# Optimization experiments

Hardware: AMD Instinct MI355X
Metric: run time of the kernel (lower is better)

The kernel has to match this reference:

```python
import jax, jax.numpy as jnp
import numpy as np

B, S, D, H = 4, 2048, 1024, 16
DH = D // H


def setup_inputs() -> dict:
    key = jax.random.key(0)
    ks = jax.random.split(key, 7)
    return {
        "Q": jax.random.normal(ks[0], (B, S, D), dtype=jnp.float32),
        "K": jax.random.normal(ks[1], (B, S, D), dtype=jnp.float32),
        "V": jax.random.normal(ks[2], (B, S, D), dtype=jnp.float32),
        "q_proj": jax.random.normal(ks[3], (D, D), dtype=jnp.float32),
        "k_proj": jax.random.normal(ks[4], (D, D), dtype=jnp.float32),
        "v_proj": jax.random.normal(ks[5], (D, D), dtype=jnp.float32),
        "output_proj": jax.random.normal(ks[6], (D, D), dtype=jnp.float32),
        "casual": 1,
    }


def reference(Q, K, V, q_proj, k_proj, v_proj, output_proj, casual):
    # projections: einsum('... a b, ... s b -> ... s a') == x @ W.T
    q = jnp.einsum('bsd,ad->bsa', Q, q_proj)
    k = jnp.einsum('bsd,ad->bsa', K, k_proj)
    v = jnp.einsum('bsd,ad->bsa', V, v_proj)
    # split heads: [B, S, H, DH]
    q = q.reshape(B, S, H, DH)
    k = k.reshape(B, S, H, DH)
    v = v.reshape(B, S, H, DH)
    # scores [B, H, Sq, Sk]
    scores = jnp.einsum('bqhd,bkhd->bhqk', q, k) / np.sqrt(DH).astype(np.float32)
    # causal mask: 0 on lower triangle, -inf above
    causal_mask = jnp.where(
        jnp.tril(jnp.ones((S, S), dtype=bool)), 0.0, -jnp.inf
    ).astype(scores.dtype)
    scores = scores + causal_mask
    attn = jax.nn.softmax(scores, axis=-1)
    # weighted values -> [B, Sq, H, DH] -> [B, Sq, D]
    out = jnp.einsum('bhqk,bkhd->bqhd', attn, v).reshape(B, S, D)
    # output projection: einsum('... a b, ... b -> ... a') == x @ W.T
    return jnp.einsum('bsd,ad->bsa', out, output_proj)
```

## Files before the change

kernel.cpp:

```cpp
#include <hip/hip_runtime.h>


typedef __attribute__((ext_vector_type(8))) _Float16 half8;
typedef __attribute__((ext_vector_type(4))) float f32x4;

#define DEVI static __device__ __forceinline__

static constexpr int cB = 4, cS = 2048, cD = 1024, cH = 16, cDH = 64;
static constexpr int cM = cB * cS;

DEVI unsigned short h2b(_Float16 h) { union { _Float16 f; unsigned short u; } x; x.f = h; return x.u; }

DEVI void async16(const void* g, void* l) {
#if defined(__HIP_DEVICE_COMPILE__)
  __builtin_amdgcn_global_load_lds((const __attribute__((address_space(1))) unsigned int*)g,
                                   (__attribute__((address_space(3))) unsigned int*)l, 16, 0, 0);
#endif
}

__global__ void split_f16_kernel(const float* __restrict__ in, unsigned short* __restrict__ hi,
                                 unsigned short* __restrict__ lo, int n) {
  int i = (blockIdx.x * blockDim.x + threadIdx.x) * 4;
  if (i >= n) return;
  float4 v = *(const float4*)(in + i);
  _Float16 h0 = (_Float16)v.x, h1 = (_Float16)v.y, h2 = (_Float16)v.z, h3 = (_Float16)v.w;
  unsigned short th[4] = {h2b(h0), h2b(h1), h2b(h2), h2b(h3)};
  *(uint2*)(hi + i) = *(const uint2*)th;
  if (lo != nullptr) {
    unsigned short tl[4] = {h2b((_Float16)(v.x - (float)h0)), h2b((_Float16)(v.y - (float)h1)),
                            h2b((_Float16)(v.z - (float)h2)), h2b((_Float16)(v.w - (float)h3))};
    *(uint2*)(lo + i) = *(const uint2*)tl;
  }
}

template <int PASSES, int OUTMODE, bool A32>
__global__ __launch_bounds__(256, 2) void gemm_bt(const void* __restrict__ Ap,
                                                  const unsigned short* __restrict__ Bh,
                                                  const unsigned short* __restrict__ Bl,
                                                  void* __restrict__ C0, void* __restrict__ C1,
                                                  int M, int N, int K) {
  __shared__ float sA32[A32 ? 128 * 32 : 1];
  __shared__ unsigned short sA16[A32 ? 1 : 128 * 32];
  __shared__ unsigned short sBh[128 * 32];
  __shared__ unsigned short sBl[(PASSES == 3) ? 128 * 32 : 1];

  const int tid = threadIdx.x, lane = tid & 63, wave = tid >> 6;
  const int wm = wave >> 1, wn = wave & 1;
  const int nb = N >> 7;
  const int bm = blockIdx.x / nb, bn = blockIdx.x % nb;
  const long r0 = (long)bm * 128, c0 = (long)bn * 128;
  const int quad = lane >> 4, cl = lane & 15;

  f32x4 acc[4][4];
#pragma unroll
  for (int mt = 0; mt < 4; ++mt)
#pragma unroll
    for (int nt = 0; nt < 4; ++nt) acc[mt][nt] = f32x4{0.f, 0.f, 0.f, 0.f};

  const int lrow8 = lane >> 3, lg8 = lane & 7;
  const int lrow16 = lane >> 2, lg4 = lane & 3;

  const float* A32p = (const float*)Ap;
  const unsigned short* A16p = (const unsigned short*)Ap;

  for (int k0 = 0; k0 < K; k0 += 32) {
    __syncthreads();
    if constexpr (A32) {
#pragma unroll
      for (int c = 0; c < 4; ++c) {
        int cc = wave * 4 + c;
        int r = cc * 8 + lrow8;
        const float* g = A32p + (r0 + r) * (long)K + k0 + ((lg8 ^ lrow8) * 4);
        async16(g, sA32 + cc * 256);
      }
    } else {
#pragma unroll
      for (int c = 0; c < 2; ++c) {
        int cc = wave * 2 + c;
        int r = cc * 16 + lrow16;
        const unsigned short* g =
            A16p + (r0 + r) * (long)K + k0 + ((lg4 ^ ((lrow16 >> 1) & 3)) * 8);
        async16(g, sA16 + cc * 512);
      }
    }
#pragma unroll
    for (int c = 0; c < 2; ++c) {
      int cc = wave * 2 + c;
      int r = cc * 16 + lrow16;
      long gb = (c0 + r) * (long)K + k0 + ((lg4 ^ ((lrow16 >> 1) & 3)) * 8);
      async16(Bh + gb, sBh + cc * 512);
      if constexpr (PASSES == 3) async16(Bl + gb, sBl + cc * 512);
    }
    __syncthreads();

    half8 ah[4], al[4], bh8[4], bl8[4];
    if constexpr (A32) {
#pragma unroll
      for (int mt = 0; mt < 4; ++mt) {
        int r = wm * 64 + mt * 16 + cl;
        int s0 = (quad * 2 + 0) ^ (r & 7), s1 = (quad * 2 + 1) ^ (r & 7);
        float fa[8];
        *(float4*)(fa) = *(const float4*)(sA32 + r * 32 + s0 * 4);
        *(float4*)(fa + 4) = *(const float4*)(sA32 + r * 32 + s1 * 4);
#pragma unroll
        for (int j = 0; j < 8; ++j) {
          _Float16 h = (_Float16)fa[j];
          ah[mt][j] = h;
          if constexpr (PASSES == 3) al[mt][j] = (_Float16)(fa[j] - (float)h);
        }
      }
    } else {
#pragma unroll
      for (int mt = 0; mt < 4; ++mt) {
        int r = wm * 64 + mt * 16 + cl;
        int s = quad ^ ((r >> 1) & 3);
        ah[mt] = *(const half8*)(sA16 + r * 32 + s * 8);
      }
    }
#pragma unroll
    for (int nt = 0; nt < 4; ++nt) {
      int r = wn * 64 + nt * 16 + cl;
      int s = quad ^ ((r >> 1) & 3);
      bh8[nt] = *(const half8*)(sBh + r * 32 + s * 8);
      if constexpr (PASSES == 3) bl8[nt] = *(const half8*)(sBl + r * 32 + s * 8);
    }
#pragma unroll
    for (int mt = 0; mt < 4; ++mt)
#pragma unroll
      for (int nt = 0; nt < 4; ++nt) {
        acc[mt][nt] = __builtin_amdgcn_mfma_f32_16x16x32_f16(ah[mt], bh8[nt], acc[mt][nt], 0, 0, 0);
        if constexpr (PASSES == 3) {
          acc[mt][nt] = __builtin_amdgcn_mfma_f32_16x16x32_f16(ah[mt], bl8[nt], acc[mt][nt], 0, 0, 0);
          acc[mt][nt] = __builtin_amdgcn_mfma_f32_16x16x32_f16(al[mt], bh8[nt], acc[mt][nt], 0, 0, 0);
        }
      }
  }

#pragma unroll
  for (int mt = 0; mt < 4; ++mt)
#pragma unroll
    for (int nt = 0; nt < 4; ++nt)
#pragma unroll
      for (int i = 0; i < 4; ++i) {
        long row = r0 + wm * 64 + mt * 16 + quad * 4 + i;
        long col = c0 + wn * 64 + nt * 16 + cl;
        float v = acc[mt][nt][i];
        if constexpr (OUTMODE == 2) {
          ((float*)C0)[row * N + col] = v;
        } else if constexpr (OUTMODE == 0) {
          ((unsigned short*)C0)[row * N + col] = h2b((_Float16)v);
        } else {
          _Float16 h = (_Float16)v;
          ((unsigned short*)C0)[row * N + col] = h2b(h);
          ((unsigned short*)C1)[row * N + col] = h2b((_Float16)(v - (float)h));
        }
      }
}

__global__ __launch_bounds__(256, 2) void flash_kernel(
    const unsigned short* __restrict__ qh_g, const unsigned short* __restrict__ ql_g,
    const unsigned short* __restrict__ kh_g, const unsigned short* __restrict__ kl_g,
    const unsigned short* __restrict__ vp_g, unsigned short* __restrict__ out) {
  __shared__ unsigned short sKh[64 * 64];
  __shared__ unsigned short sKl[64 * 64];
  __shared__ unsigned short sVt[64 * 72];
  __shared__ unsigned short sP[4][32 * 40];

  const int tid = threadIdx.x, lane = tid & 63, wave = tid >> 6;
  const int quad = lane >> 4, cl = lane & 15;
  const int qt = blockIdx.x & 15;
  const int h = (blockIdx.x >> 4) & 15;
  const int b = blockIdx.x >> 8;
  const long rowbase = (long)b * cS;
  const int q0 = qt * 128;

  half8 qh[2][2], ql[2][2];
#pragma unroll
  for (int ks = 0; ks < 2; ++ks)
#pragma unroll
    for (int mt = 0; mt < 2; ++mt) {
      long r = rowbase + q0 + wave * 32 + mt * 16 + cl;
      long off = r * cD + h * 64 + ks * 32 + quad * 8;
      qh[ks][mt] = *(const half8*)(qh_g + off);
      ql[ks][mt] = *(const half8*)(ql_g + off);
    }

  f32x4 O[2][4];
  float mrow[2][4], lrow[2][4];
#pragma unroll
  for (int mt = 0; mt < 2; ++mt) {
#pragma unroll
    for (int dt = 0; dt < 4; ++dt) O[mt][dt] = f32x4{0.f, 0.f, 0.f, 0.f};
#pragma unroll
    for (int i = 0; i < 4; ++i) { mrow[mt][i] = -1e30f; lrow[mt][i] = 0.f; }
  }

  const int lrow8 = lane >> 3, lg8 = lane & 7;
  const int kimax = 2 * qt + 1;
  for (int ki = 0; ki <= kimax; ++ki) {
    __syncthreads();
#pragma unroll
    for (int c = 0; c < 2; ++c) {
      int cc = wave * 2 + c;
      int r = cc * 8 + lrow8;
      long g = (rowbase + ki * 64 + r) * (long)cD + h * 64 + ((lg8 ^ lrow8) * 8);
      async16(kh_g + g, sKh + cc * 512);
      async16(kl_g + g, sKl + cc * 512);
    }
    {
      int r = tid >> 2, dh0 = (tid & 3) * 16;
      const unsigned short* gv = vp_g + (rowbase + ki * 64 + r) * (long)cD + h * 64 + dh0;
      unsigned short buf[16];
      *(uint4*)(buf) = *(const uint4*)(gv);
      *(uint4*)(buf + 8) = *(const uint4*)(gv + 8);
#pragma unroll
      for (int j = 0; j < 16; ++j) sVt[(dh0 + j) * 72 + r] = buf[j];
    }
    __syncthreads();

    f32x4 sacc[2][4];
#pragma unroll
    for (int mt = 0; mt < 2; ++mt)
#pragma unroll
      for (int nt = 0; nt < 4; ++nt) sacc[mt][nt] = f32x4{0.f, 0.f, 0.f, 0.f};
#pragma unroll
    for (int ks = 0; ks < 2; ++ks) {
      half8 kh8[4], kl8[4];
#pragma unroll
      for (int nt = 0; nt < 4; ++nt) {
        int r = nt * 16 + cl;
        int off = r * 64 + (((ks * 4 + quad) ^ (r & 7)) * 8);
        kh8[nt] = *(const half8*)(sKh + off);
        kl8[nt] = *(const half8*)(sKl + off);
      }
#pragma unroll
      for (int mt = 0; mt < 2; ++mt)
#pragma unroll
        for (int nt = 0; nt < 4; ++nt) {
          sacc[mt][nt] = __builtin_amdgcn_mfma_f32_16x16x32_f16(qh[ks][mt], kh8[nt], sacc[mt][nt], 0, 0, 0);
          sacc[mt][nt] = __builtin_amdgcn_mfma_f32_16x16x32_f16(qh[ks][mt], kl8[nt], sacc[mt][nt], 0, 0, 0);
          sacc[mt][nt] = __builtin_amdgcn_mfma_f32_16x16x32_f16(ql[ks][mt], kh8[nt], sacc[mt][nt], 0, 0, 0);
        }
    }
    const bool need_mask = (ki >= 2 * qt);
#pragma unroll
    for (int mt = 0; mt < 2; ++mt)
#pragma unroll
      for (int nt = 0; nt < 4; ++nt)
#pragma unroll
        for (int i = 0; i < 4; ++i) {
          float s = sacc[mt][nt][i] * 0.125f;
          if (need_mask) {
            int rg = q0 + wave * 32 + mt * 16 + quad * 4 + i;
            int cg = ki * 64 + nt * 16 + cl;
            if (cg > rg) s = -1e30f;
          }
          sacc[mt][nt][i] = s;
        }
    float alpha[2][4];
#pragma unroll
    for (int mt = 0; mt < 2; ++mt)
#pragma unroll
      for (int i = 0; i < 4; ++i) {
        float mx = sacc[mt][0][i];
#pragma unroll
        for (int nt = 1; nt < 4; ++nt) mx = fmaxf(mx, sacc[mt][nt][i]);
#pragma unroll
        for (int d = 1; d < 16; d <<= 1) mx = fmaxf(mx, __shfl_xor(mx, d));
        float mnew = fmaxf(mrow[mt][i], mx);
        float a = __expf(mrow[mt][i] - mnew);
        mrow[mt][i] = mnew;
        alpha[mt][i] = a;
        float rs = 0.f;
#pragma unroll
        for (int nt = 0; nt < 4; ++nt) {
          float p = __expf(sacc[mt][nt][i] - mnew);
          sacc[mt][nt][i] = p;
          rs += p;
        }
#pragma unroll
        for (int d = 1; d < 16; d <<= 1) rs += __shfl_xor(rs, d);
        lrow[mt][i] = lrow[mt][i] * a + rs;
      }
#pragma unroll
    for (int mt = 0; mt < 2; ++mt)
#pragma unroll
      for (int dt = 0; dt < 4; ++dt)
#pragma unroll
        for (int i = 0; i < 4; ++i) O[mt][dt][i] *= alpha[mt][i];

    unsigned short* sPw = sP[wave];
#pragma unroll
    for (int kc = 0; kc < 2; ++kc) {
#pragma unroll
      for (int mt = 0; mt < 2; ++mt)
#pragma unroll
        for (int ntl = 0; ntl < 2; ++ntl) {
          int nt = kc * 2 + ntl;
#pragma unroll
          for (int i = 0; i < 4; ++i)
            sPw[(mt * 16 + quad * 4 + i) * 40 + ntl * 16 + cl] = h2b((_Float16)sacc[mt][nt][i]);
        }
      half8 pa[2], vb[4];
#pragma unroll
      for (int mt = 0; mt < 2; ++mt)
        pa[mt] = *(const half8*)(sPw + (mt * 16 + cl) * 40 + quad * 8);
#pragma unroll
      for (int dt = 0; dt < 4; ++dt)
        vb[dt] = *(const half8*)(sVt + (dt * 16 + cl) * 72 + kc * 32 + quad * 8);
#pragma unroll
      for (int mt = 0; mt < 2; ++mt)
#pragma unroll
        for (int dt = 0; dt < 4; ++dt)
          O[mt][dt] = __builtin_amdgcn_mfma_f32_16x16x32_f16(pa[mt], vb[dt], O[mt][dt], 0, 0, 0);
    }
  }

#pragma unroll
  for (int mt = 0; mt < 2; ++mt)
#pragma unroll
    for (int dt = 0; dt < 4; ++dt)
#pragma unroll
      for (int i = 0; i < 4; ++i) {
        long r = rowbase + q0 + wave * 32 + mt * 16 + quad * 4 + i;
        out[r * cD + h * 64 + dt * 16 + cl] = h2b((_Float16)(O[mt][dt][i] / lrow[mt][i]));
      }
}

extern "C" void kernel_launch(void* const* d_in, const int* in_sizes, int n_in,
                              void* d_out, int out_size, void* d_ws, size_t ws_size,
                              hipStream_t stream) {
  const float* Q = (const float*)d_in[0];
  const float* K = (const float*)d_in[1];
  const float* V = (const float*)d_in[2];
  const float* Wq = (const float*)d_in[3];
  const float* Wk = (const float*)d_in[4];
  const float* Wv = (const float*)d_in[5];
  const float* Wo = (const float*)d_in[6];

  unsigned short* ws = (unsigned short*)d_ws;
  const size_t WD = (size_t)cD * cD;
  const size_t WM = (size_t)cM * cD;
  unsigned short* Wqh = ws;
  unsigned short* Wql = Wqh + WD;
  unsigned short* Wkh = Wql + WD;
  unsigned short* Wkl = Wkh + WD;
  unsigned short* Wvh = Wkl + WD;
  unsigned short* Woh = Wvh + WD;
  unsigned short* qph = Woh + WD;
  unsigned short* qpl = qph + WM;
  unsigned short* kph = qpl + WM;
  unsigned short* kpl = kph + WM;
  unsigned short* vp  = kpl + WM;
  unsigned short* attnb = vp + WM;

  const int nW = (int)WD;
  split_f16_kernel<<<nW / 1024, 256, 0, stream>>>(Wq, Wqh, Wql, nW);
  split_f16_kernel<<<nW / 1024, 256, 0, stream>>>(Wk, Wkh, Wkl, nW);
  split_f16_kernel<<<nW / 1024, 256, 0, stream>>>(Wv, Wvh, nullptr, nW);
  split_f16_kernel<<<nW / 1024, 256, 0, stream>>>(Wo, Woh, nullptr, nW);

  const int gblk = (cM / 128) * (cD / 128);
  gemm_bt<3, 1, true><<<gblk, 256, 0, stream>>>(Q, Wqh, Wql, qph, qpl, cM, cD, cD);
  gemm_bt<3, 1, true><<<gblk, 256, 0, stream>>>(K, Wkh, Wkl, kph, kpl, cM, cD, cD);
  gemm_bt<1, 0, true><<<gblk, 256, 0, stream>>>(V, Wvh, nullptr, vp, nullptr, cM, cD, cD);

  flash_kernel<<<cB * cH * (cS / 128), 256, 0, stream>>>(qph, qpl, kph, kpl, vp, attnb);

  gemm_bt<1, 2, false><<<gblk, 256, 0, stream>>>(attnb, Woh, nullptr, d_out, nullptr, cM, cD, cD);
}
```

Before: 581.9 us.

## Pair causal query tiles per block and streamline flash softmax bookkeeping

Each flash block now handles two query tiles (qt and 15-qt), so every block does about the same causal work, and the grid is halved. Several softmax-side tweaks come with it. The 1/8 scale is folded into Q in fp16, and the row sum comes from an extra MFMA against a ones vector instead of shuffle reductions. Rescaling of O is skipped when no row max changes, V is transposed into packed 32-bit LDS words, and masked tiles are peeled out of the main loop. Launch bounds rise to 3 blocks per CU, which risks register pressure, and pre-scaling Q in fp16 adds a little rounding.

```diff
diff --git a/kernel.cpp b/kernel.cpp
--- a/kernel.cpp
+++ b/kernel.cpp
@@ -104,9 +104,9 @@
         *(float4*)(fa + 4) = *(const float4*)(sA32 + r * 32 + s1 * 4);
 #pragma unroll
         for (int j = 0; j < 8; ++j) {
-          _Float16 h = (_Float16)fa[j];
-          ah[mt][j] = h;
-          if constexpr (PASSES == 3) al[mt][j] = (_Float16)(fa[j] - (float)h);
+          _Float16 hh = (_Float16)fa[j];
+          ah[mt][j] = hh;
+          if constexpr (PASSES == 3) al[mt][j] = (_Float16)(fa[j] - (float)hh);
         }
       }
     } else {
@@ -150,181 +150,203 @@
         } else if constexpr (OUTMODE == 0) {
           ((unsigned short*)C0)[row * N + col] = h2b((_Float16)v);
         } else {
-          _Float16 h = (_Float16)v;
-          ((unsigned short*)C0)[row * N + col] = h2b(h);
-          ((unsigned short*)C1)[row * N + col] = h2b((_Float16)(v - (float)h));
-        }
-      }
-}
-
-__global__ __launch_bounds__(256, 2) void flash_kernel(
+          _Float16 hh = (_Float16)v;
+          ((unsigned short*)C0)[row * N + col] = h2b(hh);
+          ((unsigned short*)C1)[row * N + col] = h2b((_Float16)(v - (float)hh));
+        }
+      }
+}
+
+__global__ __launch_bounds__(256, 3) void flash_kernel(
     const unsigned short* __restrict__ qh_g, const unsigned short* __restrict__ ql_g,
     const unsigned short* __restrict__ kh_g, const unsigned short* __restrict__ kl_g,
     const unsigned short* __restrict__ vp_g, unsigned short* __restrict__ out) {
   __shared__ unsigned short sKh[64 * 64];
   __shared__ unsigned short sKl[64 * 64];
-  __shared__ unsigned short sVt[64 * 72];
+  __shared__ unsigned int sVtU[64 * 34];
   __shared__ unsigned short sP[4][32 * 40];
 
   const int tid = threadIdx.x, lane = tid & 63, wave = tid >> 6;
   const int quad = lane >> 4, cl = lane & 15;
-  const int qt = blockIdx.x & 15;
-  const int h = (blockIdx.x >> 4) & 15;
-  const int b = blockIdx.x >> 8;
+  const int qp = blockIdx.x & 7;
+  const int h = (blockIdx.x >> 3) & 15;
+  const int b = blockIdx.x >> 7;
   const long rowbase = (long)b * cS;
-  const int q0 = qt * 128;
-
-  half8 qh[2][2], ql[2][2];
-#pragma unroll
-  for (int ks = 0; ks < 2; ++ks)
+  const int lrow8 = lane >> 3, lg8 = lane & 7;
+
+  for (int phase = 0; phase < 2; ++phase) {
+    const int qt = phase ? qp : (15 - qp);
+    const int q0 = qt * 128;
+
+    half8 qh[2][2], ql[2][2];
+    const _Float16 s8 = (_Float16)0.125f;
+#pragma unroll
+    for (int ks = 0; ks < 2; ++ks)
+#pragma unroll
+      for (int mt = 0; mt < 2; ++mt) {
+        long r = rowbase + q0 + wave * 32 + mt * 16 + cl;
+        long off = r * cD + h * 64 + ks * 32 + quad * 8;
+        qh[ks][mt] = *(const half8*)(qh_g + off) * s8;
+        ql[ks][mt] = *(const half8*)(ql_g + off) * s8;
+      }
+
+    f32x4 O[2][5];
+    float mrow[2][4];
 #pragma unroll
     for (int mt = 0; mt < 2; ++mt) {
-      long r = rowbase + q0 + wave * 32 + mt * 16 + cl;
-      long off = r * cD + h * 64 + ks * 32 + quad * 8;
-      qh[ks][mt] = *(const half8*)(qh_g + off);
-      ql[ks][mt] = *(const half8*)(ql_g + off);
-    }
-
-  f32x4 O[2][4];
-  float mrow[2][4], lrow[2][4];
-#pragma unroll
-  for (int mt = 0; mt < 2; ++mt) {
-#pragma unroll
-    for (int dt = 0; dt < 4; ++dt) O[mt][dt] = f32x4{0.f, 0.f, 0.f, 0.f};
-#pragma unroll
-    for (int i = 0; i < 4; ++i) { mrow[mt][i] = -1e30f; lrow[mt][i] = 0.f; }
+#pragma unroll
+      for (int dt = 0; dt < 5; ++dt) O[mt][dt] = f32x4{0.f, 0.f, 0.f, 0.f};
+#pragma unroll
+      for (int i = 0; i < 4; ++i) mrow[mt][i] = -1e30f;
+    }
+
+    half8 vone;
+#pragma unroll
+    for (int j = 0; j < 8; ++j) vone[j] = (cl == 0) ? (_Float16)1.0f : (_Float16)0.0f;
+
+    auto tile = [&](int ki, bool MASK) {
+      __syncthreads();
+#pragma unroll
+      for (int c = 0; c < 2; ++c) {
+        int cc = wave * 2 + c;
+        int r = cc * 8 + lrow8;
+        long g = (rowbase + ki * 64 + r) * (long)cD + h * 64 + ((lg8 ^ lrow8) * 8);
+        async16(kh_g + g, sKh + cc * 512);
+        async16(kl_g + g, sKl + cc * 512);
+      }
+      {
+        int r2 = tid & 31, dc = (tid >> 5) * 8;
+        const unsigned short* gv = vp_g + (rowbase + ki * 64 + 2 * r2) * (long)cD + h * 64 + dc;
+        unsigned short a[8], bb[8];
+        *(uint4*)a = *(const uint4*)gv;
+        *(uint4*)bb = *(const uint4*)(gv + cD);
+#pragma unroll
+        for (int j = 0; j < 8; ++j)
+          sVtU[(dc + j) * 34 + r2] = (unsigned int)a[j] | ((unsigned int)bb[j] << 16);
+      }
+      __syncthreads();
+
+      f32x4 sacc[2][4];
+#pragma unroll
+      for (int mt = 0; mt < 2; ++mt)
+#pragma unroll
+        for (int nt = 0; nt < 4; ++nt) sacc[mt][nt] = f32x4{0.f, 0.f, 0.f, 0.f};
+#pragma unroll
+      for (int ks = 0; ks < 2; ++ks) {
+        half8 kh8[4], kl8[4];
+#pragma unroll
+        for (int nt = 0; nt < 4; ++nt) {
+          int r = nt * 16 + cl;
+          int off = r * 64 + (((ks * 4 + quad) ^ (r & 7)) * 8);
+          kh8[nt] = *(const half8*)(sKh + off);
+          kl8[nt] = *(const half8*)(sKl + off);
+        }
+#pragma unroll
+        for (int mt = 0; mt < 2; ++mt)
+#pragma unroll
+          for (int nt = 0; nt < 4; ++nt) {
+            sacc[mt][nt] = __builtin_amdgcn_mfma_f32_16x16x32_f16(qh[ks][mt], kh8[nt], sacc[mt][nt], 0, 0, 0);
+            sacc[mt][nt] = __builtin_amdgcn_mfma_f32_16x16x32_f16(qh[ks][mt], kl8[nt], sacc[mt][nt], 0, 0, 0);
+            sacc[mt][nt] = __builtin_amdgcn_mfma_f32_16x16x32_f16(ql[ks][mt], kh8[nt], sacc[mt][nt], 0, 0, 0);
+          }
+      }
+      if (MASK) {
+#pragma unroll
+        for (int mt = 0; mt < 2; ++mt)
+#pragma unroll
+          for (int nt = 0; nt < 4; ++nt)
+#pragma unroll
+            for (int i = 0; i < 4; ++i) {
+              int rg = q0 + wave * 32 + mt * 16 + quad * 4 + i;
+              int cg = ki * 64 + nt * 16 + cl;
+              if (cg > rg) sacc[mt][nt][i] = -1e30f;
+            }
+      }
+      float mnew[2][4];
+      bool ch = false;
+#pragma unroll
+      for (int mt = 0; mt < 2; ++mt)
+#pragma unroll
+        for (int i = 0; i < 4; ++i) {
+          float mx = fmaxf(fmaxf(sacc[mt][0][i], sacc[mt][1][i]),
+                           fmaxf(sacc[mt][2][i], sacc[mt][3][i]));
+#pragma unroll
+          for (int d = 1; d < 16; d <<= 1) mx = fmaxf(mx, __shfl_xor(mx, d));
+          ch |= (mx > mrow[mt][i]);
+          mnew[mt][i] = fmaxf(mrow[mt][i], mx);
+        }
+      if (__ballot(ch)) {
+#pragma unroll
+        for (int mt = 0; mt < 2; ++mt)
+#pragma unroll
+          for (int i = 0; i < 4; ++i) {
+            float a = __expf(mrow[mt][i] - mnew[mt][i]);
+#pragma unroll
+            for (int dt = 0; dt < 5; ++dt) O[mt][dt][i] *= a;
+          }
+      }
+#pragma unroll
+      for (int mt = 0; mt < 2; ++mt)
+#pragma unroll
+        for (int i = 0; i < 4; ++i) mrow[mt][i] = mnew[mt][i];
+
+      unsigned short* sPw = sP[wave];
+#pragma unroll
+      for (int kc = 0; kc < 2; ++kc) {
+#pragma unroll
+        for (int mt = 0; mt < 2; ++mt)
+#pragma unroll
+          for (int ntl = 0; ntl < 2; ++ntl) {
+            int nt = kc * 2 + ntl;
+#pragma unroll
+            for (int i = 0; i < 4; ++i) {
+              float p = __expf(sacc[mt][nt][i] - mrow[mt][i]);
+              sPw[(mt * 16 + quad * 4 + i) * 40 + ntl * 16 + cl] = h2b((_Float16)p);
+            }
+          }
+        half8 pa[2], vb[4];
+#pragma unroll
+        for (int mt = 0; mt < 2; ++mt)
+          pa[mt] = *(const half8*)(sPw + (mt * 16 + cl) * 40 + quad * 8);
+#pragma unroll
+        for (int dt = 0; dt < 4; ++dt) {
+          int base = (dt * 16 + cl) * 34 + kc * 16 + quad * 4;
+          union { uint4 u; half8 hh; } cvt;
+          uint2 p0 = *(const uint2*)(sVtU + base);
+          uint2 p1 = *(const uint2*)(sVtU + base + 2);
+          cvt.u = uint4{p0.x, p0.y, p1.x, p1.y};
+          vb[dt] = cvt.hh;
+        }
+#pragma unroll
+        for (int mt = 0; mt < 2; ++mt) {
+#pragma unroll
+          for (int dt = 0; dt < 4; ++dt)
+            O[mt][dt] = __builtin_amdgcn_mfma_f32_16x16x32_f16(pa[mt], vb[dt], O[mt][dt], 0, 0, 0);
+          O[mt][4] = __builtin_amdgcn_mfma_f32_16x16x32_f16(pa[mt], vone, O[mt][4], 0, 0, 0);
+        }
+      }
+    };
+
+    const int full = 2 * qt;
+    for (int ki = 0; ki < full; ++ki) tile(ki, false);
+    tile(full, true);
+    tile(full + 1, true);
+
+    float lv[2][4];
+#pragma unroll
+    for (int mt = 0; mt < 2; ++mt)
+#pragma unroll
+      for (int i = 0; i < 4; ++i) lv[mt][i] = __shfl(O[mt][4][i], (lane & 48));
+#pragma unroll
+    for (int mt = 0; mt < 2; ++mt)
+#pragma unroll
+      for (int dt = 0; dt < 4; ++dt)
+#pragma unroll
+        for (int i = 0; i < 4; ++i) {
+          long r = rowbase + q0 + wave * 32 + mt * 16 + quad * 4 + i;
+          out[r * cD + h * 64 + dt * 16 + cl] = h2b((_Float16)(O[mt][dt][i] / lv[mt][i]));
+        }
   }
-
-  const int lrow8 = lane >> 3, lg8 = lane & 7;
-  const int kimax = 2 * qt + 1;
-  for (int ki = 0; ki <= kimax; ++ki) {
-    __syncthreads();
-#pragma unroll
-    for (int c = 0; c < 2; ++c) {
-      int cc = wave * 2 + c;
-      int r = cc * 8 + lrow8;
-      long g = (rowbase + ki * 64 + r) * (long)cD + h * 64 + ((lg8 ^ lrow8) * 8);
-      async16(kh_g + g, sKh + cc * 512);
-      async16(kl_g + g, sKl + cc * 512);
-    }
-    {
-      int r = tid >> 2, dh0 = (tid & 3) * 16;
-      const unsigned short* gv = vp_g + (rowbase + ki * 64 + r) * (long)cD + h * 64 + dh0;
-      unsigned short buf[16];
-      *(uint4*)(buf) = *(const uint4*)(gv);
-      *(uint4*)(buf + 8) = *(const uint4*)(gv + 8);
-#pragma unroll
-      for (int j = 0; j < 16; ++j) sVt[(dh0 + j) * 72 + r] = buf[j];
-    }
-    __syncthreads();
-
-    f32x4 sacc[2][4];
-#pragma unroll
-    for (int mt = 0; mt < 2; ++mt)
-#pragma unroll
-      for (int nt = 0; nt < 4; ++nt) sacc[mt][nt] = f32x4{0.f, 0.f, 0.f, 0.f};
-#pragma unroll
-    for (int ks = 0; ks < 2; ++ks) {
-      half8 kh8[4], kl8[4];
-#pragma unroll
-      for (int nt = 0; nt < 4; ++nt) {
-        int r = nt * 16 + cl;
-        int off = r * 64 + (((ks * 4 + quad) ^ (r & 7)) * 8);
-        kh8[nt] = *(const half8*)(sKh + off);
-        kl8[nt] = *(const half8*)(sKl + off);
-      }
-#pragma unroll
-      for (int mt = 0; mt < 2; ++mt)
-#pragma unroll
-        for (int nt = 0; nt < 4; ++nt) {
-          sacc[mt][nt] = __builtin_amdgcn_mfma_f32_16x16x32_f16(qh[ks][mt], kh8[nt], sacc[mt][nt], 0, 0, 0);
-          sacc[mt][nt] = __builtin_amdgcn_mfma_f32_16x16x32_f16(qh[ks][mt], kl8[nt], sacc[mt][nt], 0, 0, 0);
-          sacc[mt][nt] = __builtin_amdgcn_mfma_f32_16x16x32_f16(ql[ks][mt], kh8[nt], sacc[mt][nt], 0, 0, 0);
-        }
-    }
-    const bool need_mask = (ki >= 2 * qt);
-#pragma unroll
-    for (int mt = 0; mt < 2; ++mt)
-#pragma unroll
-      for (int nt = 0; nt < 4; ++nt)
-#pragma unroll
-        for (int i = 0; i < 4; ++i) {
-          float s = sacc[mt][nt][i] * 0.125f;
-          if (need_mask) {
-            int rg = q0 + wave * 32 + mt * 16 + quad * 4 + i;
-            int cg = ki * 64 + nt * 16 + cl;
-            if (cg > rg) s = -1e30f;
-          }
-          sacc[mt][nt][i] = s;
-        }
-    float alpha[2][4];
-#pragma unroll
-    for (int mt = 0; mt < 2; ++mt)
-#pragma unroll
-      for (int i = 0; i < 4; ++i) {
-        float mx = sacc[mt][0][i];
-#pragma unroll
-        for (int nt = 1; nt < 4; ++nt) mx = fmaxf(mx, sacc[mt][nt][i]);
-#pragma unroll
-        for (int d = 1; d < 16; d <<= 1) mx = fmaxf(mx, __shfl_xor(mx, d));
-        float mnew = fmaxf(mrow[mt][i], mx);
-        float a = __expf(mrow[mt][i] - mnew);
-        mrow[mt][i] = mnew;
-        alpha[mt][i] = a;
-        float rs = 0.f;
-#pragma unroll
-        for (int nt = 0; nt < 4; ++nt) {
-          float p = __expf(sacc[mt][nt][i] - mnew);
-          sacc[mt][nt][i] = p;
-          rs += p;
-        }
-#pragma unroll
-        for (int d = 1; d < 16; d <<= 1) rs += __shfl_xor(rs, d);
-        lrow[mt][i] = lrow[mt][i] * a + rs;
-      }
-#pragma unroll
-    for (int mt = 0; mt < 2; ++mt)
-#pragma unroll
-      for (int dt = 0; dt < 4; ++dt)
-#pragma unroll
-        for (int i = 0; i < 4; ++i) O[mt][dt][i] *= alpha[mt][i];
-
-    unsigned short* sPw = sP[wave];
-#pragma unroll
-    for (int kc = 0; kc < 2; ++kc) {
-#pragma unroll
-      for (int mt = 0; mt < 2; ++mt)
-#pragma unroll
-        for (int ntl = 0; ntl < 2; ++ntl) {
-          int nt = kc * 2 + ntl;
-#pragma unroll
-          for (int i = 0; i < 4; ++i)
-            sPw[(mt * 16 + quad * 4 + i) * 40 + ntl * 16 + cl] = h2b((_Float16)sacc[mt][nt][i]);
-        }
-      half8 pa[2], vb[4];
-#pragma unroll
-      for (int mt = 0; mt < 2; ++mt)
-        pa[mt] = *(const half8*)(sPw + (mt * 16 + cl) * 40 + quad * 8);
-#pragma unroll
-      for (int dt = 0; dt < 4; ++dt)
-        vb[dt] = *(const half8*)(sVt + (dt * 16 + cl) * 72 + kc * 32 + quad * 8);
-#pragma unroll
-      for (int mt = 0; mt < 2; ++mt)
-#pragma unroll
-        for (int dt = 0; dt < 4; ++dt)
-          O[mt][dt] = __builtin_amdgcn_mfma_f32_16x16x32_f16(pa[mt], vb[dt], O[mt][dt], 0, 0, 0);
-    }
-  }
-
-#pragma unroll
-  for (int mt = 0; mt < 2; ++mt)
-#pragma unroll
-    for (int dt = 0; dt < 4; ++dt)
-#pragma unroll
-      for (int i = 0; i < 4; ++i) {
-        long r = rowbase + q0 + wave * 32 + mt * 16 + quad * 4 + i;
-        out[r * cD + h * 64 + dt * 16 + cl] = h2b((_Float16)(O[mt][dt][i] / lrow[mt][i]));
-      }
 }
 
 extern "C" void kernel_launch(void* const* d_in, const int* in_sizes, int n_in,
@@ -351,7 +373,7 @@
   unsigned short* qpl = qph + WM;
   unsigned short* kph = qpl + WM;
   unsigned short* kpl = kph + WM;
-  unsigned short* vp  = kpl + WM;
+  unsigned short* vp = kpl + WM;
   unsigned short* attnb = vp + WM;
 
   const int nW = (int)WD;
@@ -365,7 +387,7 @@
   gemm_bt<3, 1, true><<<gblk, 256, 0, stream>>>(K, Wkh, Wkl, kph, kpl, cM, cD, cD);
   gemm_bt<1, 0, true><<<gblk, 256, 0, stream>>>(V, Wvh, nullptr, vp, nullptr, cM, cD, cD);
 
-  flash_kernel<<<cB * cH * (cS / 128), 256, 0, stream>>>(qph, qpl, kph, kpl, vp, attnb);
+  flash_kernel<<<cB * cH * 8, 256, 0, stream>>>(qph, qpl, kph, kpl, vp, attnb);
 
   gemm_bt<1, 2, false><<<gblk, 256, 0, stream>>>(attnb, Woh, nullptr, d_out, nullptr, cM, cD, cD);
 }
```

Result: faster. 539.8 us (-7.2%).
